# Kernel tuning notes

Hardware: AMD Instinct MI355X
Metric: run time of the kernel (lower is better)

The kernel has to match this reference:

```python
import jax, jax.numpy as jnp
import numpy as np

ALPHA = 0.2
NEG_INF = -9e15


def setup_inputs() -> dict:
    key = jax.random.key(0)
    k1, k2, k3, k4 = jax.random.split(key, 4)
    B, N, Fin, Fout = 8, 2048, 128, 64
    h = jax.random.normal(k1, (B, N, Fin), dtype=jnp.float32)
    adj = jax.random.randint(k2, (N, N), 0, 2, dtype=jnp.int32)
    # xavier-uniform-ish scale for params
    W = jax.random.normal(k3, (Fin, Fout), dtype=jnp.float32) * (1.414 * (2.0 / (Fin + Fout)) ** 0.5)
    a = jax.random.normal(k4, (2 * Fout, 1), dtype=jnp.float32) * (1.414 * (2.0 / (2 * Fout + 1)) ** 0.5)
    return {"h": h, "adj": adj, "W": W, "a": a}


def reference(h, adj, W, a):
    # h: [B,N,Fin], adj: [N,N] int, W: [Fin,Fout], a: [2*Fout,1]
    Wh = jnp.matmul(h, W)                       # [B,N,F]
    Fout = W.shape[1]
    a1 = a[:Fout, 0]                            # attends to source node i
    a2 = a[Fout:, 0]                            # attends to target node j
    # e[b,i,j] = leakyrelu(Wh[b,i]·a1 + Wh[b,j]·a2)  (no [B,N,N,2F] tensor)
    si = jnp.einsum('bnf,f->bn', Wh, a1)        # [B,N]
    sj = jnp.einsum('bnf,f->bn', Wh, a2)        # [B,N]
    e = si[:, :, None] + sj[:, None, :]         # [B,N,N]
    e = jnp.where(e > 0, e, ALPHA * e)          # leaky_relu
    mask = (adj > 0)[None, :, :]                # [1,N,N] broadcast over batch
    attention = jax.nn.softmax(jnp.where(mask, e, NEG_INF), axis=2)
    h_prime = jnp.matmul(attention, Wh)         # [B,N,F]
    return jax.nn.elu(h_prime), attention
```

## Files before the change

kernel.cpp:

```cpp
#include <hip/hip_runtime.h>
#include <hip/hip_bf16.h>
#include <string.h>

constexpr int B_ = 8;
constexpr int N_ = 2048;
constexpr int FIN = 128;
constexpr int FOUT = 64;
constexpr float ALPHA_ = 0.2f;
constexpr float NEG_INF_ = -9000000000000000.0f;

typedef __attribute__((ext_vector_type(8))) short bf16x8;
typedef __attribute__((ext_vector_type(4))) float f32x4;

static __device__ __forceinline__ unsigned short f2bf(float x) {
  unsigned int u = __float_as_uint(x);
  unsigned int r = u + 0x7fffu + ((u >> 16) & 1u);
  return (unsigned short)(r >> 16);
}

__global__ __launch_bounds__(256) void k_wh(
    const float* __restrict__ h, const float* __restrict__ W,
    const float* __restrict__ a, unsigned short* __restrict__ WhT,
    float* __restrict__ si, float* __restrict__ sj) {
  const int lane = threadIdx.x & 63;
  const int wv = threadIdx.x >> 6;
  const int grow0 = blockIdx.x * 32 + wv * 8;
  const int f = lane;
  float acc[8] = {0.f, 0.f, 0.f, 0.f, 0.f, 0.f, 0.f, 0.f};
  const float* hp = h + (size_t)grow0 * FIN;
#pragma unroll 4
  for (int k = 0; k < FIN; k += 4) {
    float w0 = W[k * FOUT + f];
    float w1 = W[(k + 1) * FOUT + f];
    float w2 = W[(k + 2) * FOUT + f];
    float w3 = W[(k + 3) * FOUT + f];
#pragma unroll
    for (int r = 0; r < 8; ++r) {
      float4 hv = *(const float4*)(hp + r * FIN + k);
      acc[r] = fmaf(hv.x, w0, acc[r]);
      acc[r] = fmaf(hv.y, w1, acc[r]);
      acc[r] = fmaf(hv.z, w2, acc[r]);
      acc[r] = fmaf(hv.w, w3, acc[r]);
    }
  }
  const float a1 = a[f], a2 = a[FOUT + f];
#pragma unroll
  for (int r = 0; r < 8; ++r) {
    float p1 = acc[r] * a1;
    float p2 = acc[r] * a2;
#pragma unroll
    for (int off = 32; off; off >>= 1) {
      p1 += __shfl_xor(p1, off);
      p2 += __shfl_xor(p2, off);
    }
    if (lane == 0) {
      si[grow0 + r] = p1;
      sj[grow0 + r] = p2;
    }
  }
  const int b = grow0 >> 11;
  const int n0 = grow0 & (N_ - 1);
  __align__(16) unsigned short u[8];
#pragma unroll
  for (int r = 0; r < 8; ++r) u[r] = f2bf(acc[r]);
  *(bf16x8*)&WhT[(((size_t)(b * FOUT + f)) << 11) + n0] = *(const bf16x8*)u;
}

__global__ __launch_bounds__(256) void k_pack(
    const int* __restrict__ adj, unsigned long long* __restrict__ mask_rm,
    unsigned int* __restrict__ mask_t) {
  const int lane = threadIdx.x & 63;
  const int wv = threadIdx.x >> 6;
  const int r = blockIdx.x * 4 + wv;
  const int* row = adj + (size_t)r * N_;
  unsigned int wacc = 0;
#pragma unroll
  for (int it = 0; it < 32; ++it) {
    int v = row[it * 64 + lane];
    unsigned long long bm = __ballot(v > 0);
    if (lane == 0) mask_rm[r * 32 + it] = bm;
    wacc |= ((unsigned int)(v > 0)) << it;
  }
  mask_t[r * 64 + lane] = wacc;
}

__global__ __launch_bounds__(256) void k_stats(
    const unsigned int* __restrict__ mask_t, const float* __restrict__ si,
    const float* __restrict__ sj, float* __restrict__ mrow,
    float* __restrict__ rrow) {
  const int lane = threadIdx.x & 63;
  const int wv = threadIdx.x >> 6;
  const int row = blockIdx.x * 4 + wv;
  const int b = row >> 11;
  const int i = row & (N_ - 1);
  const unsigned int w32 = mask_t[i * 64 + lane];
  const float* sjb = sj + ((size_t)b << 11);
  float sjv[32];
  float M = -3.0e38f;
#pragma unroll
  for (int it = 0; it < 32; ++it) {
    sjv[it] = sjb[it * 64 + lane];
    if ((w32 >> it) & 1u) M = fmaxf(M, sjv[it]);
  }
#pragma unroll
  for (int off = 32; off; off >>= 1) M = fmaxf(M, __shfl_xor(M, off));
  const float siv = si[row];
  const float e0 = siv + M;
  const float m = e0 > 0.f ? e0 : ALPHA_ * e0;
  float s = 0.f;
#pragma unroll
  for (int it = 0; it < 32; ++it) {
    float e = siv + sjv[it];
    float v = e > 0.f ? e : ALPHA_ * e;
    float p = __expf(v - m);
    s += ((w32 >> it) & 1u) ? p : 0.f;
  }
#pragma unroll
  for (int off = 32; off; off >>= 1) s += __shfl_xor(s, off);
  if (lane == 0) {
    mrow[row] = m;
    rrow[row] = 1.f / s;
  }
}

constexpr int TI = 32;
constexpr int CH = 128;

__global__ __launch_bounds__(512) void k_main(
    const unsigned short* __restrict__ WhT,
    const unsigned long long* __restrict__ mask_rm,
    const float* __restrict__ si, const float* __restrict__ sjg,
    const float* __restrict__ mrow, const float* __restrict__ rrow,
    float* __restrict__ att_out, float* __restrict__ h_out) {
  __shared__ __align__(16) unsigned short A_lds[TI * CH];
  __shared__ __align__(16) unsigned short Bt_lds[FOUT * CH];
  __shared__ float s_sj[N_];
  __shared__ float s_si[TI], s_m[TI], s_r[TI];

  const int bid = blockIdx.x;
  const int swz = (bid & 7) * 64 + (bid >> 3);
  const int b = swz >> 6;
  const int i0 = (swz & 63) * TI;

  const int tid = threadIdx.x;
  const int lane = tid & 63;
  const int wv = tid >> 6;
  const int rt = wv >> 2;
  const int ct = wv & 3;

  const unsigned char* maskb = (const unsigned char*)mask_rm;
  char* Ab = (char*)A_lds;
  char* Bb = (char*)Bt_lds;

  for (int x = tid; x < N_; x += 512) s_sj[x] = sjg[(b << 11) + x];
  if (tid < TI) {
    s_si[tid] = si[(b << 11) + i0 + tid];
    s_m[tid] = mrow[(b << 11) + i0 + tid];
    s_r[tid] = rrow[(b << 11) + i0 + tid];
  }
  __syncthreads();

  f32x4 acc = {0.f, 0.f, 0.f, 0.f};

  const int r = tid >> 4;
  const int q = tid & 15;

  for (int j0 = 0; j0 < N_; j0 += CH) {
#pragma unroll
    for (int p = 0; p < 2; ++p) {
      const int fr = (tid >> 4) + p * 32;
      bf16x8 v = *(const bf16x8*)&WhT[(((size_t)(b * FOUT + fr)) << 11) + j0 + q * 8];
      *(bf16x8*)(Bb + ((fr * 256 + q * 16) ^ ((fr & 7) << 4))) = v;
    }
    {
      const int jb = j0 + q * 8;
      const unsigned int mbits = maskb[(i0 + r) * 256 + (jb >> 3)];
      const float sir = s_si[r], mr = s_m[r], rr = s_r[r];
      const float4 sj0 = *(const float4*)&s_sj[jb];
      const float4 sj1 = *(const float4*)&s_sj[jb + 4];
      const float sjl[8] = {sj0.x, sj0.y, sj0.z, sj0.w, sj1.x, sj1.y, sj1.z, sj1.w};
      float av[8];
#pragma unroll
      for (int e = 0; e < 8; ++e) {
        float ev = sir + sjl[e];
        float v = ev > 0.f ? ev : ALPHA_ * ev;
        float p = __expf(v - mr) * rr;
        av[e] = ((mbits >> e) & 1u) ? p : 0.f;
      }
      float* ao = att_out + (((size_t)((b << 11) + i0 + r)) << 11) + jb;
      *(float4*)ao = make_float4(av[0], av[1], av[2], av[3]);
      *(float4*)(ao + 4) = make_float4(av[4], av[5], av[6], av[7]);
      __align__(16) unsigned short u[8];
#pragma unroll
      for (int e = 0; e < 8; ++e) u[e] = f2bf(av[e]);
      *(bf16x8*)(Ab + ((r * 256 + q * 16) ^ ((r & 7) << 4))) = *(const bf16x8*)u;
    }
    __syncthreads();
    {
      const int arow = rt * 16 + (lane & 15);
      const int brow = ct * 16 + (lane & 15);
      const int kb = (lane >> 4) * 16;
      const int axor = (arow & 7) << 4;
      const int bxor = (brow & 7) << 4;
#pragma unroll
      for (int ks = 0; ks < 4; ++ks) {
        bf16x8 af = *(const bf16x8*)(Ab + ((arow * 256 + ks * 64 + kb) ^ axor));
        bf16x8 bv = *(const bf16x8*)(Bb + ((brow * 256 + ks * 64 + kb) ^ bxor));
        acc = __builtin_amdgcn_mfma_f32_16x16x32_bf16(af, bv, acc, 0, 0, 0);
      }
    }
    __syncthreads();
  }

  const int colb = ct * 16 + (lane & 15);
  const int rowb = i0 + rt * 16 + ((lane >> 4) << 2);
#pragma unroll
  for (int qq = 0; qq < 4; ++qq) {
    float x = acc[qq];
    float o = x > 0.f ? x : __expf(x) - 1.f;
    h_out[(((size_t)((b << 11) + rowb + qq)) << 6) + colb] = o;
  }
}

extern "C" void kernel_launch(void* const* d_in, const int* in_sizes, int n_in,
                              void* d_out, int out_size, void* d_ws, size_t ws_size,
                              hipStream_t stream) {
  const float* h = (const float*)d_in[0];
  const int* adj = (const int*)d_in[1];
  const float* W = (const float*)d_in[2];
  const float* a = (const float*)d_in[3];

  float* out = (float*)d_out;
  float* h_out = out;
  float* att_out = out + (size_t)B_ * N_ * FOUT;

  unsigned short* WhT = (unsigned short*)d_ws;
  float* si = (float*)((char*)d_ws + (size_t)2 * 1024 * 1024);
  float* sj = si + B_ * N_;
  float* mrow = sj + B_ * N_;
  float* rrow = mrow + B_ * N_;
  unsigned long long* mask_rm = (unsigned long long*)(rrow + B_ * N_);
  unsigned int* mask_t = (unsigned int*)((char*)mask_rm + (size_t)N_ * 32 * 8);

  k_wh<<<B_ * N_ / 32, 256, 0, stream>>>(h, W, a, WhT, si, sj);
  k_pack<<<N_ / 4, 256, 0, stream>>>(adj, mask_rm, mask_t);
  k_stats<<<B_ * N_ / 4, 256, 0, stream>>>(mask_t, si, sj, mrow, rrow);
  k_main<<<B_ * N_ / TI, 512, 0, stream>>>(WhT, mask_rm, si, sj, mrow, rrow,
                                           att_out, h_out);
}
```

Before: 80.14 us.

## Compute attention fragments in registers and drop LDS staging in main kernel

```diff
diff --git a/kernel.cpp b/kernel.cpp
--- a/kernel.cpp
+++ b/kernel.cpp
@@ -123,102 +123,95 @@
   }
 }
 
-constexpr int TI = 32;
-constexpr int CH = 128;
-
 __global__ __launch_bounds__(512) void k_main(
     const unsigned short* __restrict__ WhT,
     const unsigned long long* __restrict__ mask_rm,
     const float* __restrict__ si, const float* __restrict__ sjg,
     const float* __restrict__ mrow, const float* __restrict__ rrow,
     float* __restrict__ att_out, float* __restrict__ h_out) {
-  __shared__ __align__(16) unsigned short A_lds[TI * CH];
-  __shared__ __align__(16) unsigned short Bt_lds[FOUT * CH];
-  __shared__ float s_sj[N_];
-  __shared__ float s_si[TI], s_m[TI], s_r[TI];
-
   const int bid = blockIdx.x;
-  const int swz = (bid & 7) * 64 + (bid >> 3);
-  const int b = swz >> 6;
-  const int i0 = (swz & 63) * TI;
+  const int b = bid & 7;
+  const int i0 = (bid >> 3) * 64;
 
   const int tid = threadIdx.x;
   const int lane = tid & 63;
   const int wv = tid >> 6;
-  const int rt = wv >> 2;
-  const int ct = wv & 3;
-
-  const unsigned char* maskb = (const unsigned char*)mask_rm;
-  char* Ab = (char*)A_lds;
-  char* Bb = (char*)Bt_lds;
-
-  for (int x = tid; x < N_; x += 512) s_sj[x] = sjg[(b << 11) + x];
-  if (tid < TI) {
-    s_si[tid] = si[(b << 11) + i0 + tid];
-    s_m[tid] = mrow[(b << 11) + i0 + tid];
-    s_r[tid] = rrow[(b << 11) + i0 + tid];
-  }
-  __syncthreads();
-
-  f32x4 acc = {0.f, 0.f, 0.f, 0.f};
-
-  const int r = tid >> 4;
-  const int q = tid & 15;
-
-  for (int j0 = 0; j0 < N_; j0 += CH) {
-#pragma unroll
-    for (int p = 0; p < 2; ++p) {
-      const int fr = (tid >> 4) + p * 32;
-      bf16x8 v = *(const bf16x8*)&WhT[(((size_t)(b * FOUT + fr)) << 11) + j0 + q * 8];
-      *(bf16x8*)(Bb + ((fr * 256 + q * 16) ^ ((fr & 7) << 4))) = v;
-    }
-    {
-      const int jb = j0 + q * 8;
-      const unsigned int mbits = maskb[(i0 + r) * 256 + (jb >> 3)];
-      const float sir = s_si[r], mr = s_m[r], rr = s_r[r];
-      const float4 sj0 = *(const float4*)&s_sj[jb];
-      const float4 sj1 = *(const float4*)&s_sj[jb + 4];
-      const float sjl[8] = {sj0.x, sj0.y, sj0.z, sj0.w, sj1.x, sj1.y, sj1.z, sj1.w};
+  const int rt = wv & 3;
+  const int dup = wv >> 2;
+  const int rl = lane & 15;
+  const int hi = lane >> 4;
+
+  const int row = i0 + rt * 16 + rl;
+  const int grow = (b << 11) + row;
+  const float sir = si[grow];
+  const float mK = mrow[grow] * 1.44269504f;
+  const float rr = rrow[grow];
+  const float* __restrict__ sjb = sjg + ((size_t)b << 11);
+  const unsigned char* __restrict__ maskb =
+      (const unsigned char*)mask_rm + row * 256;
+
+  const int f0 = dup * 32 + rl;
+  const int f1 = f0 + 16;
+  const unsigned short* __restrict__ wb0 = WhT + (((size_t)(b * FOUT + f0)) << 11);
+  const unsigned short* __restrict__ wb1 = WhT + (((size_t)(b * FOUT + f1)) << 11);
+
+  f32x4 acc0 = {0.f, 0.f, 0.f, 0.f};
+  f32x4 acc1 = {0.f, 0.f, 0.f, 0.f};
+
+  for (int t = 0; t < N_ / 128; ++t) {
+    const int j0 = t * 128;
+    const uint4 mr = *(const uint4*)(maskb + (j0 >> 3));
+    const unsigned int mw[4] = {mr.x, mr.y, mr.z, mr.w};
+    bf16x8 afr[4];
+
+#pragma unroll
+    for (int ks = 0; ks < 4; ++ks) {
+      const int jb = j0 + ks * 32 + hi * 8;
+      const float4 s0 = *(const float4*)(sjb + jb);
+      const float4 s1 = *(const float4*)(sjb + jb + 4);
+      const unsigned int mby = (mw[ks] >> (hi * 8)) & 0xffu;
+      const float sjl[8] = {s0.x, s0.y, s0.z, s0.w, s1.x, s1.y, s1.z, s1.w};
       float av[8];
 #pragma unroll
       for (int e = 0; e < 8; ++e) {
         float ev = sir + sjl[e];
-        float v = ev > 0.f ? ev : ALPHA_ * ev;
-        float p = __expf(v - mr) * rr;
-        av[e] = ((mbits >> e) & 1u) ? p : 0.f;
+        float v = fmaxf(ev, ALPHA_ * ev);
+        float p = exp2f(fmaf(v, 1.44269504f, -mK)) * rr;
+        av[e] = ((mby >> e) & 1u) ? p : 0.f;
       }
-      float* ao = att_out + (((size_t)((b << 11) + i0 + r)) << 11) + jb;
-      *(float4*)ao = make_float4(av[0], av[1], av[2], av[3]);
-      *(float4*)(ao + 4) = make_float4(av[4], av[5], av[6], av[7]);
+      if ((ks >> 1) == dup) {
+        float* ao = att_out + (((size_t)grow) << 11) + jb;
+        *(float4*)ao = make_float4(av[0], av[1], av[2], av[3]);
+        *(float4*)(ao + 4) = make_float4(av[4], av[5], av[6], av[7]);
+      }
       __align__(16) unsigned short u[8];
 #pragma unroll
       for (int e = 0; e < 8; ++e) u[e] = f2bf(av[e]);
-      *(bf16x8*)(Ab + ((r * 256 + q * 16) ^ ((r & 7) << 4))) = *(const bf16x8*)u;
-    }
-    __syncthreads();
-    {
-      const int arow = rt * 16 + (lane & 15);
-      const int brow = ct * 16 + (lane & 15);
-      const int kb = (lane >> 4) * 16;
-      const int axor = (arow & 7) << 4;
-      const int bxor = (brow & 7) << 4;
-#pragma unroll
-      for (int ks = 0; ks < 4; ++ks) {
-        bf16x8 af = *(const bf16x8*)(Ab + ((arow * 256 + ks * 64 + kb) ^ axor));
-        bf16x8 bv = *(const bf16x8*)(Bb + ((brow * 256 + ks * 64 + kb) ^ bxor));
-        acc = __builtin_amdgcn_mfma_f32_16x16x32_bf16(af, bv, acc, 0, 0, 0);
-      }
-    }
-    __syncthreads();
-  }
-
-  const int colb = ct * 16 + (lane & 15);
-  const int rowb = i0 + rt * 16 + ((lane >> 4) << 2);
+      afr[ks] = *(const bf16x8*)u;
+    }
+
+#pragma unroll
+    for (int ks = 0; ks < 4; ++ks) {
+      const int jb = j0 + ks * 32 + hi * 8;
+      bf16x8 bv0 = *(const bf16x8*)(wb0 + jb);
+      bf16x8 bv1 = *(const bf16x8*)(wb1 + jb);
+      acc0 = __builtin_amdgcn_mfma_f32_16x16x32_bf16(afr[ks], bv0, acc0, 0, 0, 0);
+      acc1 = __builtin_amdgcn_mfma_f32_16x16x32_bf16(afr[ks], bv1, acc1, 0, 0, 0);
+    }
+  }
+
+  const int rowb = i0 + rt * 16 + hi * 4;
+  const int colb0 = dup * 32 + rl;
+  const int colb1 = colb0 + 16;
 #pragma unroll
   for (int qq = 0; qq < 4; ++qq) {
-    float x = acc[qq];
-    float o = x > 0.f ? x : __expf(x) - 1.f;
-    h_out[(((size_t)((b << 11) + rowb + qq)) << 6) + colb] = o;
+    float x0 = acc0[qq];
+    float x1 = acc1[qq];
+    float o0 = x0 > 0.f ? x0 : __expf(x0) - 1.f;
+    float o1 = x1 > 0.f ? x1 : __expf(x1) - 1.f;
+    const size_t base = ((size_t)((b << 11) + rowb + qq)) << 6;
+    h_out[base + colb0] = o0;
+    h_out[base + colb1] = o1;
   }
 }
 
@@ -245,6 +238,6 @@
   k_wh<<<B_ * N_ / 32, 256, 0, stream>>>(h, W, a, WhT, si, sj);
   k_pack<<<N_ / 4, 256, 0, stream>>>(adj, mask_rm, mask_t);
   k_stats<<<B_ * N_ / 4, 256, 0, stream>>>(mask_t, si, sj, mrow, rrow);
-  k_main<<<B_ * N_ / TI, 512, 0, stream>>>(WhT, mask_rm, si, sj, mrow, rrow,
-                                           att_out, h_out);
-}
+  k_main<<<256, 512, 0, stream>>>(WhT, mask_rm, si, sj, mrow, rrow,
+                                  att_out, h_out);
+}
```

Result: slower. 113.5 us (+41.6%).

## Split-K attention matmul across waves with register fragments and LDS reduction

Applied to the files above, without the earlier changes.

```diff
diff --git a/kernel.cpp b/kernel.cpp
--- a/kernel.cpp
+++ b/kernel.cpp
@@ -124,18 +124,14 @@
 }
 
 constexpr int TI = 32;
-constexpr int CH = 128;
-
-__global__ __launch_bounds__(512) void k_main(
+
+__global__ __launch_bounds__(512, 4) void k_main(
     const unsigned short* __restrict__ WhT,
     const unsigned long long* __restrict__ mask_rm,
     const float* __restrict__ si, const float* __restrict__ sjg,
     const float* __restrict__ mrow, const float* __restrict__ rrow,
     float* __restrict__ att_out, float* __restrict__ h_out) {
-  __shared__ __align__(16) unsigned short A_lds[TI * CH];
-  __shared__ __align__(16) unsigned short Bt_lds[FOUT * CH];
-  __shared__ float s_sj[N_];
-  __shared__ float s_si[TI], s_m[TI], s_r[TI];
+  __shared__ float red[4][TI][FOUT];
 
   const int bid = blockIdx.x;
   const int swz = (bid & 7) * 64 + (bid >> 3);
@@ -145,80 +141,122 @@
   const int tid = threadIdx.x;
   const int lane = tid & 63;
   const int wv = tid >> 6;
-  const int rt = wv >> 2;
-  const int ct = wv & 3;
+  const int rl = lane & 15;
+  const int hi = lane >> 4;
+  const int jsl = wv * 256;
+
+  const int grow0 = (b << 11) + i0 + rl;
+  const int grow1 = grow0 + 16;
+  const float sir0 = si[grow0], sir1 = si[grow1];
+  const float mK0 = mrow[grow0] * 1.44269504f, mK1 = mrow[grow1] * 1.44269504f;
+  const float rr0 = rrow[grow0], rr1 = rrow[grow1];
+  const float* __restrict__ sjb = sjg + ((size_t)b << 11);
 
   const unsigned char* maskb = (const unsigned char*)mask_rm;
-  char* Ab = (char*)A_lds;
-  char* Bb = (char*)Bt_lds;
-
-  for (int x = tid; x < N_; x += 512) s_sj[x] = sjg[(b << 11) + x];
-  if (tid < TI) {
-    s_si[tid] = si[(b << 11) + i0 + tid];
-    s_m[tid] = mrow[(b << 11) + i0 + tid];
-    s_r[tid] = rrow[(b << 11) + i0 + tid];
+  const uint4 mA0 = *(const uint4*)(maskb + (i0 + rl) * 256 + (jsl >> 3));
+  const uint4 mA1 = *(const uint4*)(maskb + (i0 + rl) * 256 + (jsl >> 3) + 16);
+  const uint4 mB0 = *(const uint4*)(maskb + (i0 + 16 + rl) * 256 + (jsl >> 3));
+  const uint4 mB1 = *(const uint4*)(maskb + (i0 + 16 + rl) * 256 + (jsl >> 3) + 16);
+  const unsigned int mw0[8] = {mA0.x, mA0.y, mA0.z, mA0.w, mA1.x, mA1.y, mA1.z, mA1.w};
+  const unsigned int mw1[8] = {mB0.x, mB0.y, mB0.z, mB0.w, mB1.x, mB1.y, mB1.z, mB1.w};
+
+  const unsigned short* wbp[4];
+#pragma unroll
+  for (int ct = 0; ct < 4; ++ct)
+    wbp[ct] = WhT + (((size_t)(b * FOUT + ct * 16 + rl)) << 11) + jsl + hi * 8;
+
+  float* ao0 = att_out + (((size_t)grow0) << 11) + jsl + hi * 8;
+  float* ao1 = att_out + (((size_t)grow1) << 11) + jsl + hi * 8;
+
+  f32x4 acc[2][4];
+#pragma unroll
+  for (int rt = 0; rt < 2; ++rt)
+#pragma unroll
+    for (int ct = 0; ct < 4; ++ct) acc[rt][ct] = (f32x4){0.f, 0.f, 0.f, 0.f};
+
+#pragma unroll
+  for (int ks = 0; ks < 8; ++ks) {
+    const int jb = jsl + ks * 32 + hi * 8;
+    const float4 s0 = *(const float4*)(sjb + jb);
+    const float4 s1 = *(const float4*)(sjb + jb + 4);
+    const float sjl[8] = {s0.x, s0.y, s0.z, s0.w, s1.x, s1.y, s1.z, s1.w};
+
+    bf16x8 afr0, afr1;
+    {
+      const unsigned int mby = (mw0[ks] >> (hi * 8)) & 0xffu;
+      float av[8];
+#pragma unroll
+      for (int e = 0; e < 8; ++e) {
+        float ev = sir0 + sjl[e];
+        float v = fmaxf(ev, ALPHA_ * ev);
+        float p = exp2f(fmaf(v, 1.44269504f, -mK0)) * rr0;
+        av[e] = ((mby >> e) & 1u) ? p : 0.f;
+      }
+      f32x4 v0 = {av[0], av[1], av[2], av[3]};
+      f32x4 v1 = {av[4], av[5], av[6], av[7]};
+      __builtin_nontemporal_store(v0, (f32x4*)(ao0 + ks * 32));
+      __builtin_nontemporal_store(v1, (f32x4*)(ao0 + ks * 32 + 4));
+      __align__(16) unsigned short u[8];
+#pragma unroll
+      for (int e = 0; e < 8; ++e) u[e] = f2bf(av[e]);
+      afr0 = *(const bf16x8*)u;
+    }
+    {
+      const unsigned int mby = (mw1[ks] >> (hi * 8)) & 0xffu;
+      float av[8];
+#pragma unroll
+      for (int e = 0; e < 8; ++e) {
+        float ev = sir1 + sjl[e];
+        float v = fmaxf(ev, ALPHA_ * ev);
+        float p = exp2f(fmaf(v, 1.44269504f, -mK1)) * rr1;
+        av[e] = ((mby >> e) & 1u) ? p : 0.f;
+      }
+      f32x4 v0 = {av[0], av[1], av[2], av[3]};
+      f32x4 v1 = {av[4], av[5], av[6], av[7]};
+      __builtin_nontemporal_store(v0, (f32x4*)(ao1 + ks * 32));
+      __builtin_nontemporal_store(v1, (f32x4*)(ao1 + ks * 32 + 4));
+      __align__(16) unsigned short u[8];
+#pragma unroll
+      for (int e = 0; e < 8; ++e) u[e] = f2bf(av[e]);
+      afr1 = *(const bf16x8*)u;
+    }
+
+#pragma unroll
+    for (int ct = 0; ct < 4; ++ct) {
+      bf16x8 bv = *(const bf16x8*)(wbp[ct] + ks * 32);
+      acc[0][ct] = __builtin_amdgcn_mfma_f32_16x16x32_bf16(afr0, bv, acc[0][ct], 0, 0, 0);
+      acc[1][ct] = __builtin_amdgcn_mfma_f32_16x16x32_bf16(afr1, bv, acc[1][ct], 0, 0, 0);
+    }
+  }
+
+  if (wv < 4) {
+#pragma unroll
+    for (int rt = 0; rt < 2; ++rt)
+#pragma unroll
+      for (int ct = 0; ct < 4; ++ct)
+#pragma unroll
+        for (int rg = 0; rg < 4; ++rg)
+          red[wv][rt * 16 + hi * 4 + rg][ct * 16 + rl] = acc[rt][ct][rg];
   }
   __syncthreads();
-
-  f32x4 acc = {0.f, 0.f, 0.f, 0.f};
-
-  const int r = tid >> 4;
-  const int q = tid & 15;
-
-  for (int j0 = 0; j0 < N_; j0 += CH) {
-#pragma unroll
-    for (int p = 0; p < 2; ++p) {
-      const int fr = (tid >> 4) + p * 32;
-      bf16x8 v = *(const bf16x8*)&WhT[(((size_t)(b * FOUT + fr)) << 11) + j0 + q * 8];
-      *(bf16x8*)(Bb + ((fr * 256 + q * 16) ^ ((fr & 7) << 4))) = v;
-    }
-    {
-      const int jb = j0 + q * 8;
-      const unsigned int mbits = maskb[(i0 + r) * 256 + (jb >> 3)];
-      const float sir = s_si[r], mr = s_m[r], rr = s_r[r];
-      const float4 sj0 = *(const float4*)&s_sj[jb];
-      const float4 sj1 = *(const float4*)&s_sj[jb + 4];
-      const float sjl[8] = {sj0.x, sj0.y, sj0.z, sj0.w, sj1.x, sj1.y, sj1.z, sj1.w};
-      float av[8];
-#pragma unroll
-      for (int e = 0; e < 8; ++e) {
-        float ev = sir + sjl[e];
-        float v = ev > 0.f ? ev : ALPHA_ * ev;
-        float p = __expf(v - mr) * rr;
-        av[e] = ((mbits >> e) & 1u) ? p : 0.f;
-      }
-      float* ao = att_out + (((size_t)((b << 11) + i0 + r)) << 11) + jb;
-      *(float4*)ao = make_float4(av[0], av[1], av[2], av[3]);
-      *(float4*)(ao + 4) = make_float4(av[4], av[5], av[6], av[7]);
-      __align__(16) unsigned short u[8];
-#pragma unroll
-      for (int e = 0; e < 8; ++e) u[e] = f2bf(av[e]);
-      *(bf16x8*)(Ab + ((r * 256 + q * 16) ^ ((r & 7) << 4))) = *(const bf16x8*)u;
-    }
-    __syncthreads();
-    {
-      const int arow = rt * 16 + (lane & 15);
-      const int brow = ct * 16 + (lane & 15);
-      const int kb = (lane >> 4) * 16;
-      const int axor = (arow & 7) << 4;
-      const int bxor = (brow & 7) << 4;
-#pragma unroll
-      for (int ks = 0; ks < 4; ++ks) {
-        bf16x8 af = *(const bf16x8*)(Ab + ((arow * 256 + ks * 64 + kb) ^ axor));
-        bf16x8 bv = *(const bf16x8*)(Bb + ((brow * 256 + ks * 64 + kb) ^ bxor));
-        acc = __builtin_amdgcn_mfma_f32_16x16x32_bf16(af, bv, acc, 0, 0, 0);
-      }
-    }
-    __syncthreads();
-  }
-
-  const int colb = ct * 16 + (lane & 15);
-  const int rowb = i0 + rt * 16 + ((lane >> 4) << 2);
-#pragma unroll
-  for (int qq = 0; qq < 4; ++qq) {
-    float x = acc[qq];
+  if (wv >= 4) {
+#pragma unroll
+    for (int rt = 0; rt < 2; ++rt)
+#pragma unroll
+      for (int ct = 0; ct < 4; ++ct)
+#pragma unroll
+        for (int rg = 0; rg < 4; ++rg)
+          red[wv - 4][rt * 16 + hi * 4 + rg][ct * 16 + rl] += acc[rt][ct][rg];
+  }
+  __syncthreads();
+
+#pragma unroll
+  for (int k = tid; k < TI * FOUT; k += 512) {
+    const int r = k >> 6;
+    const int c = k & 63;
+    float x = red[0][r][c] + red[1][r][c] + red[2][r][c] + red[3][r][c];
     float o = x > 0.f ? x : __expf(x) - 1.f;
-    h_out[(((size_t)((b << 11) + rowb + qq)) << 6) + colb] = o;
+    h_out[(((size_t)((b << 11) + i0 + r)) << 6) + c] = o;
   }
 }
 
@@ -245,6 +283,6 @@
   k_wh<<<B_ * N_ / 32, 256, 0, stream>>>(h, W, a, WhT, si, sj);
   k_pack<<<N_ / 4, 256, 0, stream>>>(adj, mask_rm, mask_t);
   k_stats<<<B_ * N_ / 4, 256, 0, stream>>>(mask_t, si, sj, mrow, rrow);
-  k_main<<<B_ * N_ / TI, 512, 0, stream>>>(WhT, mask_rm, si, sj, mrow, rrow,
-                                           att_out, h_out);
-}
+  k_main<<<B_ * (N_ / TI), 512, 0, stream>>>(WhT, mask_rm, si, sj, mrow, rrow,
+                                             att_out, h_out);
+}
```

Result: slower. 105.1 us (+31.2%).
